# Performance work log

Measured on AMD Instinct MI355X. Metric: run time of the kernel, lower is better.

## Reference

```python
import jax, jax.numpy as jnp
import numpy as np

D, ED, N, R, K, NL = 128, 256, 16, 8, 4, 3   # d_model, d_inner, d_state, dt_rank, d_conv, n_layers
B, L = 4, 1024
HID, OUT = 256, 2
EPS = 1e-5


def setup_inputs() -> dict:
    key = jax.random.key(0)
    ks = jax.random.split(key, 16)
    g = lambda k, shape, s=0.05: jax.random.normal(k, shape, dtype=jnp.float32) * s
    return {
        "x": jax.random.normal(ks[0], (B, L, D), dtype=jnp.float32),
        # Mamba params, stacked over (2 directions, NL layers)
        "rms_w": jnp.ones((2, NL, D), jnp.float32),
        "in_w": g(ks[1], (2, NL, 2 * ED, D)),
        "in_b": g(ks[2], (2, NL, 2 * ED)),
        "conv_w": g(ks[3], (2, NL, ED, K)),
        "conv_b": g(ks[4], (2, NL, ED)),
        "xproj_w": g(ks[5], (2, NL, R + 2 * N, ED)),
        "dt_w": g(ks[6], (2, NL, ED, R)),
        "dt_b": g(ks[7], (2, NL, ED)),
        "A_log": jnp.broadcast_to(jnp.log(jnp.arange(1.0, N + 1.0, dtype=jnp.float32)), (2, NL, ED, N)) + 0.0,
        "Dp": jnp.ones((2, NL, ED), jnp.float32),
        "out_w": g(ks[8], (2, NL, D, ED)),
        "out_b": g(ks[9], (2, NL, D)),
        # MLP head params (BatchNorm in training mode: batch stats)
        "bn1_g": jnp.ones((2 * D,), jnp.float32), "bn1_b": jnp.zeros((2 * D,), jnp.float32),
        "w1": g(ks[10], (HID, 2 * D)), "b1": g(ks[11], (HID,)),
        "bn2_g": jnp.ones((HID,), jnp.float32), "bn2_b": jnp.zeros((HID,), jnp.float32),
        "w2": g(ks[12], (HID, HID)), "b2": g(ks[13], (HID,)),
        "bn3_g": jnp.ones((HID,), jnp.float32), "bn3_b": jnp.zeros((HID,), jnp.float32),
        "w3": g(ks[14], (OUT, HID)), "b3": g(ks[15], (OUT,)),
    }


def _rms(x, w):
    return x * jax.lax.rsqrt(jnp.mean(x * x, axis=-1, keepdims=True) + EPS) * w


def _dwconv(x, w, b):
    # causal depthwise conv; x: (B,L,ED), w: (ED,K)
    y = jax.lax.conv_general_dilated(x.transpose(0, 2, 1), w[:, None, :], (1,), [(K - 1, 0)],
                                     feature_group_count=ED, dimension_numbers=("NCH", "OIH", "NCH"))
    return y.transpose(0, 2, 1) + b


def _ssm(dA, dBx, C):
    # dA,dBx: (B,L,ED,N); C: (B,L,N) -> y: (B,L,ED)
    def step(h, inp):
        a, bx, c = inp
        h = a * h + bx
        return h, jnp.einsum("ben,bn->be", h, c)
    h0 = jnp.zeros((dA.shape[0], ED, N), dA.dtype)
    _, ys = jax.lax.scan(step, h0, (dA.transpose(1, 0, 2, 3), dBx.transpose(1, 0, 2, 3), C.transpose(1, 0, 2)))
    return ys.transpose(1, 0, 2)


def _block(x, in_w, in_b, conv_w, conv_b, xproj_w, dt_w, dt_b, A_log, Dp, out_w, out_b):
    xz = x @ in_w.T + in_b
    xi, z = xz[..., :ED], xz[..., ED:]
    xi = jax.nn.silu(_dwconv(xi, conv_w, conv_b))
    dbc = xi @ xproj_w.T
    dt, Bm, Cm = dbc[..., :R], dbc[..., R:R + N], dbc[..., R + N:]
    delta = jax.nn.softplus(dt @ dt_w.T + dt_b)            # (B,L,ED)
    A = -jnp.exp(A_log)                                    # (ED,N)
    dA = jnp.exp(delta[..., None] * A)                     # (B,L,ED,N)
    dBx = (delta * xi)[..., None] * Bm[:, :, None, :]      # (B,L,ED,N)
    y = _ssm(dA, dBx, Cm) + Dp * xi
    y = y * jax.nn.silu(z)
    return y @ out_w.T + out_b


def _mamba(x, d, rms_w, in_w, in_b, conv_w, conv_b, xproj_w, dt_w, dt_b, A_log, Dp, out_w, out_b):
    for l in range(NL):
        x = x + _block(_rms(x, rms_w[d, l]), in_w[d, l], in_b[d, l], conv_w[d, l], conv_b[d, l],
                       xproj_w[d, l], dt_w[d, l], dt_b[d, l], A_log[d, l], Dp[d, l], out_w[d, l], out_b[d, l])
    return x


def _bn(x, g, b):
    m = jnp.mean(x, axis=0)
    v = jnp.mean((x - m) ** 2, axis=0)  # biased var, torch BN training mode
    return (x - m) * jax.lax.rsqrt(v + EPS) * g + b


def _forward(x, rms_w, in_w, in_b, conv_w, conv_b, xproj_w, dt_w, dt_b, A_log, Dp, out_w, out_b,
             bn1_g, bn1_b, w1, b1, bn2_g, bn2_b, w2, b2, bn3_g, bn3_b, w3, b3):
    mp = (rms_w, in_w, in_b, conv_w, conv_b, xproj_w, dt_w, dt_b, A_log, Dp, out_w, out_b)
    fwd = _mamba(x, 0, *mp)
    bwd = jnp.flip(_mamba(jnp.flip(x, axis=1), 1, *mp), axis=1)
    h = jnp.concatenate([fwd, bwd], axis=2).reshape(B * L, 2 * D)
    h = jax.nn.leaky_relu(_bn(h, bn1_g, bn1_b) @ w1.T + b1)
    h = jax.nn.leaky_relu(_bn(h, bn2_g, bn2_b) @ w2.T + b2)
    h = _bn(h, bn3_g, bn3_b) @ w3.T + b3
    return h.reshape(B, L, OUT)


def reference(x, rms_w, in_w, in_b, conv_w, conv_b, xproj_w, dt_w, dt_b, A_log, Dp, out_w, out_b,
              bn1_g, bn1_b, w1, b1, bn2_g, bn2_b, w2, b2, bn3_g, bn3_b, w3, b3):
    return _forward(x, rms_w, in_w, in_b, conv_w, conv_b, xproj_w, dt_w, dt_b, A_log, Dp, out_w, out_b,
                    bn1_g, bn1_b, w1, b1, bn2_g, bn2_b, w2, b2, bn3_g, bn3_b, w3, b3)
```

## Files before the change

kernel.cpp:

```cpp
#include <hip/hip_runtime.h>
#include <hip/hip_bf16.h>

#define NL 3
#define EPS 1e-5f

#define C_RMSW   0L
#define C_INW    768L
#define C_INB    393984L
#define C_CONVW  397056L
#define C_CONVB  403200L
#define C_XPROJW 404736L
#define C_DTW    466176L
#define C_DTB    478464L
#define C_ALOG   480000L
#define C_DP     504576L
#define C_OUTW   506112L
#define C_OUTB   702720L
#define C_BN1G   703488L
#define C_BN1B   703744L
#define C_W1     704000L
#define C_B1     769536L
#define C_BN2G   769792L
#define C_BN2B   770048L
#define C_W2     770304L
#define C_B2     835840L
#define C_BN3G   836096L
#define C_BN3B   836352L
#define C_W3     836608L
#define C_B3     837120L
#define FLAG_OFF 837184L
#define X0_OFF   837248L
#define X1_OFF   1361536L
#define XZT_OFF  1885824L
#define XCP_OFF  6080128L
#define DBCT_OFF 8177280L
#define YGP_OFF  8504960L
#define BNS_OFF  10602112L
#define H1_OFF   XZT_OFF
#define H2_OFF   (XZT_OFF + 1048576L)

struct Ptrs { const void* p[25]; };

static __device__ const int  CV_SRC[26] = {0,0,1,2,3,4,5,6,7,8,9,10,11,12,13,14,15,16,17,18,19,20,21,22,23,24};
static __device__ const long CV_DST[26] = {X0_OFF,X1_OFF,C_RMSW,C_INW,C_INB,C_CONVW,C_CONVB,C_XPROJW,C_DTW,C_DTB,
                                           C_ALOG,C_DP,C_OUTW,C_OUTB,C_BN1G,C_BN1B,C_W1,C_B1,C_BN2G,C_BN2B,
                                           C_W2,C_B2,C_BN3G,C_BN3B,C_W3,C_B3};
static __device__ const int  CV_SZ[26]  = {524288,524288,768,393216,3072,6144,1536,61440,12288,1536,
                                           24576,1536,196608,768,256,256,65536,256,256,256,
                                           65536,256,256,256,512,2};

__global__ __launch_bounds__(256) void k_convert(Ptrs ps, float* __restrict__ ws) {
  bool isbf = (*(const unsigned int*)ps.p[1]) == 0x3F803F80u;
  if (blockIdx.x == 0 && blockIdx.y == 0 && threadIdx.x == 0) ws[FLAG_OFF] = isbf ? 1.f : 0.f;
  int job = blockIdx.y;
  int n = CV_SZ[job];
  const void* s = ps.p[CV_SRC[job]];
  float* dp = ws + CV_DST[job];
  int stride = gridDim.x * blockDim.x;
  bool permute = (job < 2);
  for (int i = blockIdx.x * blockDim.x + threadIdx.x; i < n; i += stride) {
    long si = i;
    if (permute) {
      int row = i >> 7, col = i & 127;
      int b = row >> 10, p = row & 1023;
      int t = ((p & 63) << 4) + (p >> 6);
      si = ((long)((b << 10) + t) << 7) + col;
    }
    float v;
    if (isbf) {
      unsigned int u = ((const unsigned short*)s)[si];
      v = __uint_as_float(u << 16);
    } else {
      v = ((const float*)s)[si];
    }
    dp[i] = v;
  }
}

#define ASLD 68

__device__ inline void mm_inner(const float* As, const float* Bs, float4* acc) {
  int tx = threadIdx.x & 15, ty = threadIdx.x >> 4;
  #pragma unroll
  for (int k = 0; k < 64; ++k) {
    float4 av = *(const float4*)&As[k*ASLD + ty*4];
    float4 bv = *(const float4*)&Bs[k*ASLD + tx*4];
    acc[0].x = fmaf(av.x,bv.x,acc[0].x); acc[0].y = fmaf(av.x,bv.y,acc[0].y); acc[0].z = fmaf(av.x,bv.z,acc[0].z); acc[0].w = fmaf(av.x,bv.w,acc[0].w);
    acc[1].x = fmaf(av.y,bv.x,acc[1].x); acc[1].y = fmaf(av.y,bv.y,acc[1].y); acc[1].z = fmaf(av.y,bv.z,acc[1].z); acc[1].w = fmaf(av.y,bv.w,acc[1].w);
    acc[2].x = fmaf(av.z,bv.x,acc[2].x); acc[2].y = fmaf(av.z,bv.y,acc[2].y); acc[2].z = fmaf(av.z,bv.z,acc[2].z); acc[2].w = fmaf(av.z,bv.w,acc[2].w);
    acc[3].x = fmaf(av.w,bv.x,acc[3].x); acc[3].y = fmaf(av.w,bv.y,acc[3].y); acc[3].z = fmaf(av.w,bv.z,acc[3].z); acc[3].w = fmaf(av.w,bv.w,acc[3].w);
  }
}

__device__ inline void stageT_g(float* S, const float* src, int ld, int row0, int k0, int nvalid) {
  int m = threadIdx.x >> 2, q = threadIdx.x & 3;
  const float* p = src + (long)(row0 + m) * ld + k0 + q*16;
  bool ok = (row0 + m) < nvalid;
  #pragma unroll
  for (int j = 0; j < 4; ++j) {
    float4 v = ok ? *(const float4*)(p + j*4) : make_float4(0.f,0.f,0.f,0.f);
    int kk = q*16 + j*4;
    S[(kk+0)*ASLD+m] = v.x; S[(kk+1)*ASLD+m] = v.y; S[(kk+2)*ASLD+m] = v.z; S[(kk+3)*ASLD+m] = v.w;
  }
}

__device__ inline void stageD(float* S, const float* srcT, long ld, int m0, int k0) {
  int k = threadIdx.x >> 2, q = threadIdx.x & 3;
  const float* p = srcT + (long)(k0 + k) * ld + m0 + q*16;
  float4 v0 = *(const float4*)(p);
  float4 v1 = *(const float4*)(p+4);
  float4 v2 = *(const float4*)(p+8);
  float4 v3 = *(const float4*)(p+12);
  float* s = &S[k*ASLD + q*16];
  *(float4*)(s)    = v0; *(float4*)(s+4)  = v1; *(float4*)(s+8)  = v2; *(float4*)(s+12) = v3;
}

__global__ __launch_bounds__(256) void k1_rms_inproj(float* __restrict__ ws, int layer) {
  int d = blockIdx.z, mt = blockIdx.x, nt = blockIdx.y;
  const float* X  = ws + (d ? X1_OFF : X0_OFF);
  const float* W  = ws + C_INW + (long)((d*NL+layer)*512) * 128;
  const float* Rw = ws + C_RMSW + (d*NL+layer)*128;
  const float* Bi = ws + C_INB + (d*NL+layer)*512;
  __shared__ float As[64*ASLD];
  __shared__ float Bs[64*ASLD];
  __shared__ float rsq[64][4];
  __shared__ float rsc[64];
  int tx = threadIdx.x & 15, ty = threadIdx.x >> 4;
  float4 acc[4] = {make_float4(0,0,0,0),make_float4(0,0,0,0),make_float4(0,0,0,0),make_float4(0,0,0,0)};
  float sq = 0.f;
  for (int kt = 0; kt < 2; ++kt) {
    int k0 = kt * 64;
    {
      int m = threadIdx.x >> 2, q = threadIdx.x & 3;
      const float* p  = X + (long)(mt*64 + m) * 128 + k0 + q*16;
      const float* rw = Rw + k0 + q*16;
      #pragma unroll
      for (int j = 0; j < 4; ++j) {
        float4 v = *(const float4*)(p + j*4);
        float4 r = *(const float4*)(rw + j*4);
        sq += v.x*v.x + v.y*v.y + v.z*v.z + v.w*v.w;
        int kk = q*16 + j*4;
        As[(kk+0)*ASLD+m] = v.x*r.x; As[(kk+1)*ASLD+m] = v.y*r.y;
        As[(kk+2)*ASLD+m] = v.z*r.z; As[(kk+3)*ASLD+m] = v.w*r.w;
      }
    }
    stageT_g(Bs, W, 128, nt*64, k0, 512);
    __syncthreads();
    mm_inner(As, Bs, acc);
    __syncthreads();
  }
  { int m = threadIdx.x >> 2, q = threadIdx.x & 3; rsq[m][q] = sq; }
  __syncthreads();
  if (threadIdx.x < 64) {
    float s = rsq[threadIdx.x][0] + rsq[threadIdx.x][1] + rsq[threadIdx.x][2] + rsq[threadIdx.x][3];
    rsc[threadIdx.x] = rsqrtf(s * (1.f/128.f) + EPS);
  }
  __syncthreads();
  int n0 = tx*4;
  float4 bb = *(const float4*)&Bi[nt*64 + n0];
  const float* bbp = (const float*)&bb;
  #pragma unroll
  for (int i = 0; i < 4; ++i) {
    int m = ty*4 + i;
    float r = rsc[m];
    const float* av = (const float*)&acc[i];
    #pragma unroll
    for (int cc = 0; cc < 4; ++cc) {
      As[(n0+cc)*65 + m] = av[cc]*r + bbp[cc];
    }
  }
  __syncthreads();
  float* xzt = ws + XZT_OFF + (long)d*2097152L + (long)(nt*64)*4096 + mt*64;
  #pragma unroll
  for (int r = 0; r < 16; ++r) {
    int el = r*256 + threadIdx.x;
    int row = el >> 6, m = el & 63;
    xzt[(long)row*4096 + m] = As[row*65 + m];
  }
}

__global__ __launch_bounds__(256) void k2_conv(float* __restrict__ ws, int layer) {
  int e = blockIdx.x, d = blockIdx.y;
  const float* xrow = ws + XZT_OFF + (long)d*2097152L + (long)e*4096;
  float* orow = ws + XCP_OFF + (long)d*1048576L + (long)e*4096;
  __shared__ float s1[4*1040];
  __shared__ float s2[4*1040];
  int tid = threadIdx.x;
  #pragma unroll
  for (int r = 0; r < 16; ++r) {
    int g = r*256 + tid;
    int b = g >> 10, p = g & 1023;
    int s = (p >> 6)*65 + (p & 63);
    s1[b*1040 + s] = xrow[g];
  }
  __syncthreads();
  float4 wv = *(const float4*)(ws + C_CONVW + (long)((d*NL+layer)*256 + e) * 4);
  float cb = ws[C_CONVB + (d*NL+layer)*256 + e];
  #pragma unroll
  for (int r = 0; r < 16; ++r) {
    int tg = r*256 + tid;
    int b = tg >> 10, tl = tg & 1023;
    const float* st = s1 + b*1040;
    #define SIDX(t) (((t)&15)*65 + ((t)>>4))
    float a = cb;
    if (d == 0) {
      float x0 = (tl >= 3) ? st[SIDX(tl-3)] : 0.f;
      float x1 = (tl >= 2) ? st[SIDX(tl-2)] : 0.f;
      float x2 = (tl >= 1) ? st[SIDX(tl-1)] : 0.f;
      float x3 = st[SIDX(tl)];
      a += wv.x*x0 + wv.y*x1 + wv.z*x2 + wv.w*x3;
    } else {
      float x0 = (tl <= 1020) ? st[SIDX(tl+3)] : 0.f;
      float x1 = (tl <= 1021) ? st[SIDX(tl+2)] : 0.f;
      float x2 = (tl <= 1022) ? st[SIDX(tl+1)] : 0.f;
      float x3 = st[SIDX(tl)];
      a += wv.x*x0 + wv.y*x1 + wv.z*x2 + wv.w*x3;
    }
    #undef SIDX
    s2[b*1040 + ((tl & 15)*65 + (tl >> 4))] = a / (1.f + __expf(-a));
  }
  __syncthreads();
  #pragma unroll
  for (int r = 0; r < 16; ++r) {
    int g = r*256 + tid;
    int b = g >> 10, p = g & 1023;
    orow[g] = s2[b*1040 + (p >> 6)*65 + (p & 63)];
  }
}

__global__ __launch_bounds__(256) void k3_xproj(float* __restrict__ ws, int layer) {
  int d = blockIdx.z, mt = blockIdx.x;
  int m0 = mt * 64;
  const float* srcT = ws + XCP_OFF + (long)d*1048576L;
  const float* W = ws + C_XPROJW + (long)((d*NL+layer)*40) * 256;
  __shared__ float As[64*ASLD];
  __shared__ float Bs[64*ASLD];
  float4 acc[4] = {make_float4(0,0,0,0),make_float4(0,0,0,0),make_float4(0,0,0,0),make_float4(0,0,0,0)};
  for (int kt = 0; kt < 4; ++kt) {
    stageD(As, srcT, 4096L, m0, kt*64);
    stageT_g(Bs, W, 256, 0, kt*64, 40);
    __syncthreads();
    mm_inner(As, Bs, acc);
    __syncthreads();
  }
  int tx = threadIdx.x & 15, ty = threadIdx.x >> 4;
  #pragma unroll
  for (int i = 0; i < 4; ++i) {
    const float* av = (const float*)&acc[i];
    #pragma unroll
    for (int cc = 0; cc < 4; ++cc) {
      Bs[(tx*4+cc)*65 + ty*4+i] = av[cc];
    }
  }
  __syncthreads();
  float* dbcT = ws + DBCT_OFF + (long)d*163840L;
  #pragma unroll
  for (int r = 0; r < 10; ++r) {
    int el = r*256 + threadIdx.x;
    int n = el >> 6, m = el & 63;
    dbcT[(long)n*4096 + m0 + m] = Bs[n*65 + m];
  }
}

__device__ inline float softplusf(float x) {
  if (x > 20.f) return x;
  return __logf(1.f + __expf(x));
}

__global__ __launch_bounds__(256) void k5_scan(float* __restrict__ ws, int layer) {
  int d = blockIdx.z, b = blockIdx.y, eg = blockIdx.x;
  int es = threadIdx.x >> 6;
  int c  = threadIdx.x & 63;
  int e = eg*4 + es;
  int g0 = b*1024 + c;
  const float* xcp = ws + XCP_OFF + (long)d*1048576L + (long)e*4096 + g0;
  const float* zp  = ws + XZT_OFF + (long)d*2097152L + (long)(256+e)*4096 + g0;
  const float* dbc = ws + DBCT_OFF + (long)d*163840L + g0;
  float*       yo  = ws + YGP_OFF + (long)d*1048576L + (long)e*4096 + g0;
  const float* dw = ws + C_DTW + (long)((d*NL+layer)*256 + e)*8;
  float dtb = ws[C_DTB + (d*NL+layer)*256 + e];
  const float* al = ws + C_ALOG + (long)((d*NL+layer)*256 + e)*16;
  float Dpe = ws[C_DP + (d*NL+layer)*256 + e];
  float dtw[8];
  #pragma unroll
  for (int n = 0; n < 8; ++n) dtw[n] = dw[n];
  float Anv[16]; bool fast = true;
  #pragma unroll
  for (int n = 0; n < 16; ++n) {
    Anv[n] = -__expf(al[n]);
    fast = fast && (fabsf(Anv[n] + (float)(n+1)) < 1e-3f * (float)(n+1));
  }
  __shared__ float aL[4*64*17];
  __shared__ float hL[4*64*17];
  float h[16], ap[16], del[16], xcv[16];
  float Q = 1.f;
  #pragma unroll
  for (int n = 0; n < 16; ++n) { h[n] = 0.f; ap[n] = 1.f; }
  int i0 = d ? 15 : 0, di = d ? -1 : 1;
  for (int s = 0; s < 16; ++s) {
    int i = i0 + s*di;
    int off = i*64;
    float a0 = dtb;
    #pragma unroll
    for (int n = 0; n < 8; ++n) a0 += dbc[(long)n*4096 + off] * dtw[n];
    float dl = softplusf(a0);
    float xc = xcp[off];
    del[s] = dl; xcv[s] = xc;
    float dx = dl * xc;
    if (fast) {
      float q = __expf(-dl);
      float qp[16];
      qp[0]=q; qp[1]=q*q; qp[2]=qp[1]*q; qp[3]=qp[1]*qp[1];
      float q4=qp[3];
      qp[4]=qp[0]*q4; qp[5]=qp[1]*q4; qp[6]=qp[2]*q4; qp[7]=q4*q4;
      float q8=qp[7];
      #pragma unroll
      for (int j = 0; j < 8; ++j) qp[8+j]=qp[j]*q8;
      Q *= q;
      #pragma unroll
      for (int n = 0; n < 16; ++n)
        h[n] = fmaf(qp[n], h[n], dx * dbc[(long)(8+n)*4096 + off]);
    } else {
      #pragma unroll
      for (int n = 0; n < 16; ++n) {
        float a = __expf(dl * Anv[n]);
        ap[n] *= a;
        h[n] = fmaf(a, h[n], dx * dbc[(long)(8+n)*4096 + off]);
      }
    }
  }
  if (fast) {
    float p = Q;
    #pragma unroll
    for (int n = 0; n < 16; ++n) { ap[n] = p; p *= Q; }
  }
  int base = (es*64 + c)*17;
  #pragma unroll
  for (int n = 0; n < 16; ++n) { aL[base+n] = ap[n]; hL[base+n] = h[n]; }
  __syncthreads();
  if (threadIdx.x < 64) {
    int e2 = threadIdx.x >> 4, n = threadIdx.x & 15;
    float h0 = 0.f;
    for (int s2 = 0; s2 < 64; ++s2) {
      int cc = d ? (63 - s2) : s2;
      int ix = (e2*64 + cc)*17 + n;
      float ta = aL[ix], th = hL[ix];
      aL[ix] = h0;
      h0 = fmaf(ta, h0, th);
    }
  }
  __syncthreads();
  #pragma unroll
  for (int n = 0; n < 16; ++n) h[n] = aL[base+n];
  for (int s = 0; s < 16; ++s) {
    int i = i0 + s*di;
    int off = i*64;
    float dl = del[s], xc = xcv[s];
    float dx = dl * xc;
    float zr = zp[off];
    float zg = zr / (1.f + __expf(-zr));
    float ya[4] = {0.f,0.f,0.f,0.f};
    if (fast) {
      float q = __expf(-dl);
      float qp[16];
      qp[0]=q; qp[1]=q*q; qp[2]=qp[1]*q; qp[3]=qp[1]*qp[1];
      float q4=qp[3];
      qp[4]=qp[0]*q4; qp[5]=qp[1]*q4; qp[6]=qp[2]*q4; qp[7]=q4*q4;
      float q8=qp[7];
      #pragma unroll
      for (int j = 0; j < 8; ++j) qp[8+j]=qp[j]*q8;
      #pragma unroll
      for (int n = 0; n < 16; ++n) {
        h[n] = fmaf(qp[n], h[n], dx * dbc[(long)(8+n)*4096 + off]);
        ya[n & 3] = fmaf(h[n], dbc[(long)(24+n)*4096 + off], ya[n & 3]);
      }
    } else {
      #pragma unroll
      for (int n = 0; n < 16; ++n) {
        float a = __expf(dl * Anv[n]);
        h[n] = fmaf(a, h[n], dx * dbc[(long)(8+n)*4096 + off]);
        ya[n & 3] = fmaf(h[n], dbc[(long)(24+n)*4096 + off], ya[n & 3]);
      }
    }
    float y = (ya[0] + ya[1]) + (ya[2] + ya[3]);
    y = fmaf(Dpe, xc, y);
    yo[off] = y * zg;
  }
}

__global__ __launch_bounds__(256) void k6_outproj(float* __restrict__ ws, int layer) {
  int d = blockIdx.z, mt = blockIdx.x, nt = blockIdx.y;
  int m0 = mt * 64;
  const float* srcT = ws + YGP_OFF + (long)d*1048576L;
  const float* W  = ws + C_OUTW + (long)((d*NL+layer)*128) * 256;
  const float* Ob = ws + C_OUTB + (d*NL+layer)*128;
  float* Xd = ws + (d ? X1_OFF : X0_OFF);
  __shared__ float As[64*ASLD];
  __shared__ float Bs[64*ASLD];
  float4 acc[4] = {make_float4(0,0,0,0),make_float4(0,0,0,0),make_float4(0,0,0,0),make_float4(0,0,0,0)};
  for (int kt = 0; kt < 4; ++kt) {
    stageD(As, srcT, 4096L, m0, kt*64);
    stageT_g(Bs, W, 256, nt*64, kt*64, 128);
    __syncthreads();
    mm_inner(As, Bs, acc);
    __syncthreads();
  }
  int tx = threadIdx.x & 15, ty = threadIdx.x >> 4;
  int n0 = nt*64 + tx*4;
  float4 ob4 = *(const float4*)&Ob[n0];
  #pragma unroll
  for (int i = 0; i < 4; ++i) {
    long tok = (long)m0 + ty*4 + i;
    float4 cur = *(float4*)&Xd[tok*128 + n0];
    float4 v;
    v.x = acc[i].x + ob4.x + cur.x; v.y = acc[i].y + ob4.y + cur.y;
    v.z = acc[i].z + ob4.z + cur.z; v.w = acc[i].w + ob4.w + cur.w;
    *(float4*)&Xd[tok*128 + n0] = v;
  }
}

__global__ __launch_bounds__(256) void bn_stats(float* __restrict__ ws, int stage) {
  int ch = blockIdx.x;
  const float* src; long ld; const float* g; const float* bb;
  if (stage == 0) { src = ws + ((ch < 128) ? (X0_OFF + ch) : (X1_OFF + ch - 128)); ld = 128; g = ws + C_BN1G; bb = ws + C_BN1B; }
  else if (stage == 1) { src = ws + H1_OFF + ch; ld = 256; g = ws + C_BN2G; bb = ws + C_BN2B; }
  else { src = ws + H2_OFF + ch; ld = 256; g = ws + C_BN3G; bb = ws + C_BN3B; }
  float s = 0.f, s2 = 0.f;
  for (int i = threadIdx.x; i < 4096; i += 256) {
    float v = src[(long)i * ld];
    s += v; s2 += v*v;
  }
  #pragma unroll
  for (int o = 32; o > 0; o >>= 1) { s += __shfl_down(s, o, 64); s2 += __shfl_down(s2, o, 64); }
  __shared__ float ls[4], ls2[4];
  int wid = threadIdx.x >> 6, lane = threadIdx.x & 63;
  if (lane == 0) { ls[wid] = s; ls2[wid] = s2; }
  __syncthreads();
  if (threadIdx.x == 0) {
    float S = ls[0]+ls[1]+ls[2]+ls[3], S2 = ls2[0]+ls2[1]+ls2[2]+ls2[3];
    float mean = S * (1.f/4096.f);
    float var = S2 * (1.f/4096.f) - mean*mean;
    float sc = g[ch] * rsqrtf(var + EPS);
    ws[BNS_OFF + stage*512 + ch] = sc;
    ws[BNS_OFF + stage*512 + 256 + ch] = bb[ch] - mean * sc;
  }
}

template<int STAGE>
__global__ __launch_bounds__(256) void hgemm_k(float* __restrict__ ws, void* dout) {
  int mt = blockIdx.x, nt = blockIdx.y;
  const float* sc = ws + BNS_OFF + STAGE*512;
  const float* sh = sc + 256;
  const float* W = ws + (STAGE == 0 ? C_W1 : (STAGE == 1 ? C_W2 : C_W3));
  __shared__ float As[64*ASLD];
  __shared__ float Bs[64*ASLD];
  float4 acc[4] = {make_float4(0,0,0,0),make_float4(0,0,0,0),make_float4(0,0,0,0),make_float4(0,0,0,0)};
  for (int kt = 0; kt < 4; ++kt) {
    int k0 = kt * 64;
    const float* src; int ld;
    if (STAGE == 0) { ld = 128; src = (k0 < 128) ? (ws + X0_OFF + k0) : (ws + X1_OFF + (k0 - 128)); }
    else { ld = 256; src = ws + (STAGE == 1 ? H1_OFF : H2_OFF) + k0; }
    {
      int m = threadIdx.x >> 2, q = threadIdx.x & 3;
      const float* p   = src + (long)(mt*64 + m) * ld + q*16;
      const float* scp = sc + k0 + q*16;
      const float* shp = sh + k0 + q*16;
      #pragma unroll
      for (int j = 0; j < 4; ++j) {
        float4 v  = *(const float4*)(p + j*4);
        float4 s4 = *(const float4*)(scp + j*4);
        float4 h4 = *(const float4*)(shp + j*4);
        int kk = q*16 + j*4;
        As[(kk+0)*ASLD+m] = v.x*s4.x + h4.x; As[(kk+1)*ASLD+m] = v.y*s4.y + h4.y;
        As[(kk+2)*ASLD+m] = v.z*s4.z + h4.z; As[(kk+3)*ASLD+m] = v.w*s4.w + h4.w;
      }
    }
    stageT_g(Bs, W, 256, nt*64, k0, STAGE == 2 ? 2 : 256);
    __syncthreads();
    mm_inner(As, Bs, acc);
    __syncthreads();
  }
  int tx = threadIdx.x & 15, ty = threadIdx.x >> 4;
  if (STAGE == 2) {
    if (tx == 0) {
      bool isbf = ws[FLAG_OFF] != 0.f;
      float b0 = ws[C_B3], b1 = ws[C_B3 + 1];
      #pragma unroll
      for (int i = 0; i < 4; ++i) {
        int r = mt*64 + ty*4 + i;
        int b = r >> 10, p = r & 1023;
        int t = ((p & 63) << 4) + (p >> 6);
        long tok = (long)(b << 10) + t;
        float v0 = acc[i].x + b0, v1 = acc[i].y + b1;
        if (isbf) {
          __hip_bfloat16* o = (__hip_bfloat16*)dout;
          o[tok*2]   = __float2bfloat16(v0);
          o[tok*2+1] = __float2bfloat16(v1);
        } else {
          float* o = (float*)dout;
          o[tok*2] = v0; o[tok*2+1] = v1;
        }
      }
    }
  } else {
    const float* bp = ws + (STAGE == 0 ? C_B1 : C_B2);
    int n0 = nt*64 + tx*4;
    float4 b4 = *(const float4*)&bp[n0];
    float* H = ws + (STAGE == 0 ? H1_OFF : H2_OFF);
    #pragma unroll
    for (int i = 0; i < 4; ++i) {
      long tok = (long)mt*64 + ty*4 + i;
      float4 v;
      v.x = acc[i].x + b4.x; v.y = acc[i].y + b4.y; v.z = acc[i].z + b4.z; v.w = acc[i].w + b4.w;
      v.x = v.x > 0.f ? v.x : 0.01f*v.x;
      v.y = v.y > 0.f ? v.y : 0.01f*v.y;
      v.z = v.z > 0.f ? v.z : 0.01f*v.z;
      v.w = v.w > 0.f ? v.w : 0.01f*v.w;
      *(float4*)&H[tok*256 + n0] = v;
    }
  }
}

extern "C" void kernel_launch(void* const* d_in, const int* in_sizes, int n_in,
                              void* d_out, int out_size, void* d_ws, size_t ws_size,
                              hipStream_t stream) {
  (void)in_sizes; (void)n_in; (void)out_size; (void)ws_size;
  float* ws = (float*)d_ws;
  Ptrs ps;
  for (int i = 0; i < 25; ++i) ps.p[i] = d_in[i];
  k_convert<<<dim3(64, 26), dim3(256), 0, stream>>>(ps, ws);
  for (int l = 0; l < NL; ++l) {
    k1_rms_inproj<<<dim3(64, 8, 2), dim3(256), 0, stream>>>(ws, l);
    k2_conv      <<<dim3(256, 2),   dim3(256), 0, stream>>>(ws, l);
    k3_xproj     <<<dim3(64, 1, 2), dim3(256), 0, stream>>>(ws, l);
    k5_scan      <<<dim3(64, 4, 2), dim3(256), 0, stream>>>(ws, l);
    k6_outproj   <<<dim3(64, 2, 2), dim3(256), 0, stream>>>(ws, l);
  }
  bn_stats<<<dim3(256), dim3(256), 0, stream>>>(ws, 0);
  hgemm_k<0><<<dim3(64, 4), dim3(256), 0, stream>>>(ws, d_out);
  bn_stats<<<dim3(256), dim3(256), 0, stream>>>(ws, 1);
  hgemm_k<1><<<dim3(64, 4), dim3(256), 0, stream>>>(ws, d_out);
  bn_stats<<<dim3(256), dim3(256), 0, stream>>>(ws, 2);
  hgemm_k<2><<<dim3(64, 1), dim3(256), 0, stream>>>(ws, d_out);
}
```

Baseline: 463.9 us.

## Fuse all stages into one persistent cooperative kernel with grid syncs

Turns the 22 separate kernel launches into one persistent cooperative kernel of 256 blocks. Each stage loops over virtual block indices and stages are separated by grid.sync(), with shared memory carved from one static buffer. The aim is to remove per-launch overhead and the gaps between kernels. In exchange, each stage runs on only 256 blocks at one block per CU, giving less latency hiding, and the grid barriers cost time. A fallback multi-kernel path runs if the cooperative launch fails.

```diff
diff --git a/kernel.cpp b/kernel.cpp
--- a/kernel.cpp
+++ b/kernel.cpp
@@ -1,5 +1,7 @@
 #include <hip/hip_runtime.h>
 #include <hip/hip_bf16.h>
+#include <hip/hip_cooperative_groups.h>
+namespace cg = cooperative_groups;
 
 #define NL 3
 #define EPS 1e-5f
@@ -49,35 +51,9 @@
                                            24576,1536,196608,768,256,256,65536,256,256,256,
                                            65536,256,256,256,512,2};
 
-__global__ __launch_bounds__(256) void k_convert(Ptrs ps, float* __restrict__ ws) {
-  bool isbf = (*(const unsigned int*)ps.p[1]) == 0x3F803F80u;
-  if (blockIdx.x == 0 && blockIdx.y == 0 && threadIdx.x == 0) ws[FLAG_OFF] = isbf ? 1.f : 0.f;
-  int job = blockIdx.y;
-  int n = CV_SZ[job];
-  const void* s = ps.p[CV_SRC[job]];
-  float* dp = ws + CV_DST[job];
-  int stride = gridDim.x * blockDim.x;
-  bool permute = (job < 2);
-  for (int i = blockIdx.x * blockDim.x + threadIdx.x; i < n; i += stride) {
-    long si = i;
-    if (permute) {
-      int row = i >> 7, col = i & 127;
-      int b = row >> 10, p = row & 1023;
-      int t = ((p & 63) << 4) + (p >> 6);
-      si = ((long)((b << 10) + t) << 7) + col;
-    }
-    float v;
-    if (isbf) {
-      unsigned int u = ((const unsigned short*)s)[si];
-      v = __uint_as_float(u << 16);
-    } else {
-      v = ((const float*)s)[si];
-    }
-    dp[i] = v;
-  }
-}
-
 #define ASLD 68
+#define NBLK 256
+#define SMEM_FLOATS 9088
 
 __device__ inline void mm_inner(const float* As, const float* Bs, float4* acc) {
   int tx = threadIdx.x & 15, ty = threadIdx.x >> 4;
@@ -115,19 +91,26 @@
   *(float4*)(s)    = v0; *(float4*)(s+4)  = v1; *(float4*)(s+8)  = v2; *(float4*)(s+12) = v3;
 }
 
-__global__ __launch_bounds__(256) void k1_rms_inproj(float* __restrict__ ws, int layer) {
-  int d = blockIdx.z, mt = blockIdx.x, nt = blockIdx.y;
+__device__ inline float softplusf(float x) {
+  if (x > 20.f) return x;
+  return __logf(1.f + __expf(x));
+}
+
+__device__ void k1_tile(float* __restrict__ ws, int layer, int vb, float* smem) {
+  int d = vb >> 9, rem = vb & 511;
+  int nt = rem >> 6, mt = rem & 63;
+  float* As = smem;
+  float* Bs = smem + 4352;
+  float* rsq = smem + 8704;
+  float* rsc = smem + 8960;
   const float* X  = ws + (d ? X1_OFF : X0_OFF);
   const float* W  = ws + C_INW + (long)((d*NL+layer)*512) * 128;
   const float* Rw = ws + C_RMSW + (d*NL+layer)*128;
   const float* Bi = ws + C_INB + (d*NL+layer)*512;
-  __shared__ float As[64*ASLD];
-  __shared__ float Bs[64*ASLD];
-  __shared__ float rsq[64][4];
-  __shared__ float rsc[64];
   int tx = threadIdx.x & 15, ty = threadIdx.x >> 4;
   float4 acc[4] = {make_float4(0,0,0,0),make_float4(0,0,0,0),make_float4(0,0,0,0),make_float4(0,0,0,0)};
   float sq = 0.f;
+  __syncthreads();
   for (int kt = 0; kt < 2; ++kt) {
     int k0 = kt * 64;
     {
@@ -149,10 +132,10 @@
     mm_inner(As, Bs, acc);
     __syncthreads();
   }
-  { int m = threadIdx.x >> 2, q = threadIdx.x & 3; rsq[m][q] = sq; }
+  { int m = threadIdx.x >> 2, q = threadIdx.x & 3; rsq[m*4+q] = sq; }
   __syncthreads();
   if (threadIdx.x < 64) {
-    float s = rsq[threadIdx.x][0] + rsq[threadIdx.x][1] + rsq[threadIdx.x][2] + rsq[threadIdx.x][3];
+    float s = rsq[threadIdx.x*4] + rsq[threadIdx.x*4+1] + rsq[threadIdx.x*4+2] + rsq[threadIdx.x*4+3];
     rsc[threadIdx.x] = rsqrtf(s * (1.f/128.f) + EPS);
   }
   __syncthreads();
@@ -179,13 +162,14 @@
   }
 }
 
-__global__ __launch_bounds__(256) void k2_conv(float* __restrict__ ws, int layer) {
-  int e = blockIdx.x, d = blockIdx.y;
+__device__ void k2_row(float* __restrict__ ws, int layer, int vb, float* smem) {
+  int e = vb & 255, d = vb >> 8;
+  float* s1 = smem;
+  float* s2 = smem + 4160;
   const float* xrow = ws + XZT_OFF + (long)d*2097152L + (long)e*4096;
   float* orow = ws + XCP_OFF + (long)d*1048576L + (long)e*4096;
-  __shared__ float s1[4*1040];
-  __shared__ float s2[4*1040];
   int tid = threadIdx.x;
+  __syncthreads();
   #pragma unroll
   for (int r = 0; r < 16; ++r) {
     int g = r*256 + tid;
@@ -228,14 +212,15 @@
   }
 }
 
-__global__ __launch_bounds__(256) void k3_xproj(float* __restrict__ ws, int layer) {
-  int d = blockIdx.z, mt = blockIdx.x;
+__device__ void k3_tile(float* __restrict__ ws, int layer, int vb, float* smem) {
+  int d = vb >> 6, mt = vb & 63;
   int m0 = mt * 64;
+  float* As = smem;
+  float* Bs = smem + 4352;
   const float* srcT = ws + XCP_OFF + (long)d*1048576L;
   const float* W = ws + C_XPROJW + (long)((d*NL+layer)*40) * 256;
-  __shared__ float As[64*ASLD];
-  __shared__ float Bs[64*ASLD];
   float4 acc[4] = {make_float4(0,0,0,0),make_float4(0,0,0,0),make_float4(0,0,0,0),make_float4(0,0,0,0)};
+  __syncthreads();
   for (int kt = 0; kt < 4; ++kt) {
     stageD(As, srcT, 4096L, m0, kt*64);
     stageT_g(Bs, W, 256, 0, kt*64, 40);
@@ -262,13 +247,11 @@
   }
 }
 
-__device__ inline float softplusf(float x) {
-  if (x > 20.f) return x;
-  return __logf(1.f + __expf(x));
-}
-
-__global__ __launch_bounds__(256) void k5_scan(float* __restrict__ ws, int layer) {
-  int d = blockIdx.z, b = blockIdx.y, eg = blockIdx.x;
+__device__ void k5_unit(float* __restrict__ ws, int layer, int vb, float* smem) {
+  int d = vb >> 8, rem = vb & 255;
+  int b = rem >> 6, eg = rem & 63;
+  float* aL = smem;
+  float* hL = smem + 4352;
   int es = threadIdx.x >> 6;
   int c  = threadIdx.x & 63;
   int e = eg*4 + es;
@@ -290,8 +273,6 @@
     Anv[n] = -__expf(al[n]);
     fast = fast && (fabsf(Anv[n] + (float)(n+1)) < 1e-3f * (float)(n+1));
   }
-  __shared__ float aL[4*64*17];
-  __shared__ float hL[4*64*17];
   float h[16], ap[16], del[16], xcv[16];
   float Q = 1.f;
   #pragma unroll
@@ -335,6 +316,7 @@
     for (int n = 0; n < 16; ++n) { ap[n] = p; p *= Q; }
   }
   int base = (es*64 + c)*17;
+  __syncthreads();
   #pragma unroll
   for (int n = 0; n < 16; ++n) { aL[base+n] = ap[n]; hL[base+n] = h[n]; }
   __syncthreads();
@@ -388,16 +370,18 @@
   }
 }
 
-__global__ __launch_bounds__(256) void k6_outproj(float* __restrict__ ws, int layer) {
-  int d = blockIdx.z, mt = blockIdx.x, nt = blockIdx.y;
+__device__ void k6_tile(float* __restrict__ ws, int layer, int vb, float* smem) {
+  int d = vb >> 7, rem = vb & 127;
+  int nt = rem >> 6, mt = rem & 63;
   int m0 = mt * 64;
+  float* As = smem;
+  float* Bs = smem + 4352;
   const float* srcT = ws + YGP_OFF + (long)d*1048576L;
   const float* W  = ws + C_OUTW + (long)((d*NL+layer)*128) * 256;
   const float* Ob = ws + C_OUTB + (d*NL+layer)*128;
   float* Xd = ws + (d ? X1_OFF : X0_OFF);
-  __shared__ float As[64*ASLD];
-  __shared__ float Bs[64*ASLD];
   float4 acc[4] = {make_float4(0,0,0,0),make_float4(0,0,0,0),make_float4(0,0,0,0),make_float4(0,0,0,0)};
+  __syncthreads();
   for (int kt = 0; kt < 4; ++kt) {
     stageD(As, srcT, 4096L, m0, kt*64);
     stageT_g(Bs, W, 256, nt*64, kt*64, 128);
@@ -419,8 +403,7 @@
   }
 }
 
-__global__ __launch_bounds__(256) void bn_stats(float* __restrict__ ws, int stage) {
-  int ch = blockIdx.x;
+__device__ void bn_ch(float* __restrict__ ws, int ch, int stage, float* smem) {
   const float* src; long ld; const float* g; const float* bb;
   if (stage == 0) { src = ws + ((ch < 128) ? (X0_OFF + ch) : (X1_OFF + ch - 128)); ld = 128; g = ws + C_BN1G; bb = ws + C_BN1B; }
   else if (stage == 1) { src = ws + H1_OFF + ch; ld = 256; g = ws + C_BN2G; bb = ws + C_BN2B; }
@@ -432,8 +415,9 @@
   }
   #pragma unroll
   for (int o = 32; o > 0; o >>= 1) { s += __shfl_down(s, o, 64); s2 += __shfl_down(s2, o, 64); }
-  __shared__ float ls[4], ls2[4];
+  float* ls = smem; float* ls2 = smem + 4;
   int wid = threadIdx.x >> 6, lane = threadIdx.x & 63;
+  __syncthreads();
   if (lane == 0) { ls[wid] = s; ls2[wid] = s2; }
   __syncthreads();
   if (threadIdx.x == 0) {
@@ -447,14 +431,15 @@
 }
 
 template<int STAGE>
-__global__ __launch_bounds__(256) void hgemm_k(float* __restrict__ ws, void* dout) {
-  int mt = blockIdx.x, nt = blockIdx.y;
+__device__ void hg_tile(float* __restrict__ ws, int vb, float* smem, void* dout) {
+  int mt = vb & 63, nt = vb >> 6;
+  float* As = smem;
+  float* Bs = smem + 4352;
   const float* sc = ws + BNS_OFF + STAGE*512;
   const float* sh = sc + 256;
   const float* W = ws + (STAGE == 0 ? C_W1 : (STAGE == 1 ? C_W2 : C_W3));
-  __shared__ float As[64*ASLD];
-  __shared__ float Bs[64*ASLD];
   float4 acc[4] = {make_float4(0,0,0,0),make_float4(0,0,0,0),make_float4(0,0,0,0),make_float4(0,0,0,0)};
+  __syncthreads();
   for (int kt = 0; kt < 4; ++kt) {
     int k0 = kt * 64;
     const float* src; int ld;
@@ -521,25 +506,123 @@
   }
 }
 
+__device__ void convert_body(const Ptrs& ps, float* __restrict__ ws, int blk, int nblk) {
+  bool isbf = (*(const unsigned int*)ps.p[1]) == 0x3F803F80u;
+  if (blk == 0 && threadIdx.x == 0) ws[FLAG_OFF] = isbf ? 1.f : 0.f;
+  for (int job = 0; job < 26; ++job) {
+    int n = CV_SZ[job];
+    const void* s = ps.p[CV_SRC[job]];
+    float* dp = ws + CV_DST[job];
+    bool permute = (job < 2);
+    for (int i = blk*256 + (int)threadIdx.x; i < n; i += nblk*256) {
+      long si = i;
+      if (permute) {
+        int row = i >> 7, col = i & 127;
+        int b = row >> 10, p = row & 1023;
+        int t = ((p & 63) << 4) + (p >> 6);
+        si = ((long)((b << 10) + t) << 7) + col;
+      }
+      float v;
+      if (isbf) {
+        unsigned int u = ((const unsigned short*)s)[si];
+        v = __uint_as_float(u << 16);
+      } else {
+        v = ((const float*)s)[si];
+      }
+      dp[i] = v;
+    }
+  }
+}
+
+__global__ __launch_bounds__(256, 1) void mega(Ptrs ps, float* __restrict__ ws, void* dout) {
+  __shared__ float smem[SMEM_FLOATS];
+  cg::grid_group grid = cg::this_grid();
+  int blk = blockIdx.x;
+  convert_body(ps, ws, blk, NBLK);
+  grid.sync();
+  for (int l = 0; l < NL; ++l) {
+    for (int vb = blk; vb < 1024; vb += NBLK) k1_tile(ws, l, vb, smem);
+    grid.sync();
+    for (int vb = blk; vb < 512; vb += NBLK) k2_row(ws, l, vb, smem);
+    grid.sync();
+    if (blk < 128) k3_tile(ws, l, blk, smem);
+    grid.sync();
+    for (int vb = blk; vb < 512; vb += NBLK) k5_unit(ws, l, vb, smem);
+    grid.sync();
+    k6_tile(ws, l, blk, smem);
+    grid.sync();
+  }
+  bn_ch(ws, blk, 0, smem);
+  grid.sync();
+  hg_tile<0>(ws, blk, smem, dout);
+  grid.sync();
+  bn_ch(ws, blk, 1, smem);
+  grid.sync();
+  hg_tile<1>(ws, blk, smem, dout);
+  grid.sync();
+  bn_ch(ws, blk, 2, smem);
+  grid.sync();
+  if (blk < 64) hg_tile<2>(ws, blk, smem, dout);
+}
+
+__global__ __launch_bounds__(256) void g_convert(Ptrs ps, float* __restrict__ ws) {
+  convert_body(ps, ws, blockIdx.x, gridDim.x);
+}
+__global__ __launch_bounds__(256) void g_k1(float* __restrict__ ws, int layer) {
+  __shared__ float smem[SMEM_FLOATS];
+  k1_tile(ws, layer, blockIdx.z*512 + blockIdx.y*64 + blockIdx.x, smem);
+}
+__global__ __launch_bounds__(256) void g_k2(float* __restrict__ ws, int layer) {
+  __shared__ float smem[SMEM_FLOATS];
+  k2_row(ws, layer, blockIdx.y*256 + blockIdx.x, smem);
+}
+__global__ __launch_bounds__(256) void g_k3(float* __restrict__ ws, int layer) {
+  __shared__ float smem[SMEM_FLOATS];
+  k3_tile(ws, layer, blockIdx.z*64 + blockIdx.x, smem);
+}
+__global__ __launch_bounds__(256) void g_k5(float* __restrict__ ws, int layer) {
+  __shared__ float smem[SMEM_FLOATS];
+  k5_unit(ws, layer, blockIdx.z*256 + blockIdx.y*64 + blockIdx.x, smem);
+}
+__global__ __launch_bounds__(256) void g_k6(float* __restrict__ ws, int layer) {
+  __shared__ float smem[SMEM_FLOATS];
+  k6_tile(ws, layer, blockIdx.z*128 + blockIdx.y*64 + blockIdx.x, smem);
+}
+__global__ __launch_bounds__(256) void g_bn(float* __restrict__ ws, int stage) {
+  __shared__ float smem[16];
+  bn_ch(ws, blockIdx.x, stage, smem);
+}
+template<int STAGE>
+__global__ __launch_bounds__(256) void g_hg(float* __restrict__ ws, void* dout) {
+  __shared__ float smem[SMEM_FLOATS];
+  hg_tile<STAGE>(ws, blockIdx.y*64 + blockIdx.x, smem, dout);
+}
+
 extern "C" void kernel_launch(void* const* d_in, const int* in_sizes, int n_in,
                               void* d_out, int out_size, void* d_ws, size_t ws_size,
                               hipStream_t stream) {
   (void)in_sizes; (void)n_in; (void)out_size; (void)ws_size;
   float* ws = (float*)d_ws;
-  Ptrs ps;
+  static Ptrs ps;
   for (int i = 0; i < 25; ++i) ps.p[i] = d_in[i];
-  k_convert<<<dim3(64, 26), dim3(256), 0, stream>>>(ps, ws);
-  for (int l = 0; l < NL; ++l) {
-    k1_rms_inproj<<<dim3(64, 8, 2), dim3(256), 0, stream>>>(ws, l);
-    k2_conv      <<<dim3(256, 2),   dim3(256), 0, stream>>>(ws, l);
-    k3_xproj     <<<dim3(64, 1, 2), dim3(256), 0, stream>>>(ws, l);
-    k5_scan      <<<dim3(64, 4, 2), dim3(256), 0, stream>>>(ws, l);
-    k6_outproj   <<<dim3(64, 2, 2), dim3(256), 0, stream>>>(ws, l);
-  }
-  bn_stats<<<dim3(256), dim3(256), 0, stream>>>(ws, 0);
-  hgemm_k<0><<<dim3(64, 4), dim3(256), 0, stream>>>(ws, d_out);
-  bn_stats<<<dim3(256), dim3(256), 0, stream>>>(ws, 1);
-  hgemm_k<1><<<dim3(64, 4), dim3(256), 0, stream>>>(ws, d_out);
-  bn_stats<<<dim3(256), dim3(256), 0, stream>>>(ws, 2);
-  hgemm_k<2><<<dim3(64, 1), dim3(256), 0, stream>>>(ws, d_out);
-}
+  void* dout = d_out;
+  void* args[] = { (void*)&ps, (void*)&ws, (void*)&dout };
+  hipError_t err = hipLaunchCooperativeKernel((void*)mega, dim3(NBLK), dim3(256),
+                                              args, 0, stream);
+  if (err != hipSuccess) {
+    g_convert<<<dim3(64), dim3(256), 0, stream>>>(ps, ws);
+    for (int l = 0; l < NL; ++l) {
+      g_k1<<<dim3(64, 8, 2), dim3(256), 0, stream>>>(ws, l);
+      g_k2<<<dim3(256, 2),   dim3(256), 0, stream>>>(ws, l);
+      g_k3<<<dim3(64, 1, 2), dim3(256), 0, stream>>>(ws, l);
+      g_k5<<<dim3(64, 4, 2), dim3(256), 0, stream>>>(ws, l);
+      g_k6<<<dim3(64, 2, 2), dim3(256), 0, stream>>>(ws, l);
+    }
+    g_bn<<<dim3(256), dim3(256), 0, stream>>>(ws, 0);
+    g_hg<0><<<dim3(64, 4), dim3(256), 0, stream>>>(ws, dout);
+    g_bn<<<dim3(256), dim3(256), 0, stream>>>(ws, 1);
+    g_hg<1><<<dim3(64, 4), dim3(256), 0, stream>>>(ws, dout);
+    g_bn<<<dim3(256), dim3(256), 0, stream>>>(ws, 2);
+    g_hg<2><<<dim3(64, 1), dim3(256), 0, stream>>>(ws, dout);
+  }
+}
```

Result: slower. 1.444 ms (+211.2%).
